# Kernel tuning notes

Measured on AMD Instinct MI355X. Metric: run time of the kernel, lower is better.

The kernel has to match this reference:

```python
import jax, jax.numpy as jnp
import numpy as np

S = 32          # input grid resolution
N = 2048        # active input voxels
C = 256         # in channels
CO = 128        # out channels
S2 = 2 * S      # upsampled resolution
M = 8 * N       # candidate child voxels
EPS = 1e-6


def setup_inputs() -> dict:
    key = jax.random.key(0)
    ks = jax.random.split(key, 8)
    # unique voxel coordinates (sparse occupancy)
    lin = jax.random.permutation(ks[0], S ** 3)[:N]
    coords = jnp.stack([lin // (S * S), (lin // S) % S, lin % S], axis=-1).astype(jnp.int32)
    sc = 0.05
    return {
        "feats": jax.random.normal(ks[1], (N, C), jnp.float32),
        "norm1_w": 1.0 + 0.1 * jax.random.normal(ks[2], (C,), jnp.float32),
        "norm1_b": 0.1 * jax.random.normal(ks[3], (C,), jnp.float32),
        "subdiv_w": sc * jax.random.normal(ks[4], (C, 8), jnp.float32),
        "subdiv_b": jnp.zeros((8,), jnp.float32),
        "conv1_w": sc * jax.random.normal(ks[5], (27, C, CO), jnp.float32),
        "conv1_b": jnp.zeros((CO,), jnp.float32),
        "conv2_w": sc * jax.random.normal(ks[6], (27, CO, CO), jnp.float32),
        "conv2_b": jnp.zeros((CO,), jnp.float32),
        "skip_w": sc * jax.random.normal(ks[7], (C, CO), jnp.float32),
        "skip_b": jnp.zeros((CO,), jnp.float32),
        "coords": coords,
    }


def _layernorm(x, w=None, b=None):
    # LayerNorm32: fp32 math, eps=1e-6
    m = jnp.mean(x, axis=-1, keepdims=True)
    v = jnp.var(x, axis=-1, keepdims=True)
    y = (x - m) * jax.lax.rsqrt(v + EPS)
    if w is not None:
        y = y * w + b
    return y


def _sparse_conv(feats, nidx, w, b):
    # submanifold 3x3x3 sparse conv: gather 27 neighbors, contract.
    # nidx: [M,27] with sentinel M pointing at a zero row.
    pad = jnp.concatenate([feats, jnp.zeros((1, feats.shape[1]), feats.dtype)], axis=0)
    g = pad[nidx]                                   # [M, 27, Cin]
    return jnp.einsum('nkc,kcd->nd', g, w) + b


def _forward(feats, norm1_w, norm1_b, subdiv_w, subdiv_b, conv1_w, conv1_b,
             conv2_w, conv2_b, skip_w, skip_b, coords):
    # subdiv prediction (SparseLinear C -> 8)
    subdiv = feats @ subdiv_w + subdiv_b            # [N, 8]
    # norm1 + silu
    h = jax.nn.silu(_layernorm(feats, norm1_w, norm1_b))
    # sparse upsample x2 with octree subdivision mask
    mask = (subdiv > 0).reshape(-1)                 # [M]
    j = jnp.arange(8, dtype=jnp.int32)
    offs8 = jnp.stack([(j >> 2) & 1, (j >> 1) & 1, j & 1], axis=-1)  # [8,3]
    cc = (coords[:, None, :] * 2 + offs8[None]).reshape(-1, 3)        # [M,3]
    h_c = jnp.where(mask[:, None], jnp.repeat(h, 8, axis=0), 0.0)     # [M,C]
    x_c = jnp.where(mask[:, None], jnp.repeat(feats, 8, axis=0), 0.0)
    # neighbor lookup grid (padded by 1; default M -> zero feature row)
    grid = jnp.full((S2 + 2, S2 + 2, S2 + 2), M, jnp.int32)
    grid = grid.at[cc[:, 0] + 1, cc[:, 1] + 1, cc[:, 2] + 1].set(
        jnp.arange(M, dtype=jnp.int32))
    d = jnp.arange(-1, 2, dtype=jnp.int32)
    offs27 = jnp.stack(jnp.meshgrid(d, d, d, indexing='ij'), axis=-1).reshape(27, 3)
    nc = cc[:, None, :] + 1 + offs27[None]          # [M,27,3]
    nidx = grid[nc[..., 0], nc[..., 1], nc[..., 2]] # [M,27]
    # conv1 -> norm2 (no affine) -> silu -> conv2
    h1 = jax.nn.silu(_layernorm(_sparse_conv(h_c, nidx, conv1_w, conv1_b)))
    h2 = _sparse_conv(h1, nidx, conv2_w, conv2_b)
    # residual with linear skip; mask out non-subdivided children
    out = (h2 + x_c @ skip_w + skip_b) * mask[:, None].astype(h2.dtype)
    return out, subdiv


def reference(feats, norm1_w, norm1_b, subdiv_w, subdiv_b, conv1_w, conv1_b,
              conv2_w, conv2_b, skip_w, skip_b, coords):
    return _forward(feats, norm1_w, norm1_b, subdiv_w, subdiv_b, conv1_w,
                    conv1_b, conv2_w, conv2_b, skip_w, skip_b, coords)
```

## Files before the change

kernel.cpp:

```cpp
#include <hip/hip_runtime.h>
#include <cstdint>
#include <cstddef>

constexpr int N  = 2048;
constexpr int C  = 256;
constexpr int CO = 128;
constexpr int M  = 16384;
constexpr int G  = 66;
constexpr int KP = 4;
constexpr int KCHUNK = 7;
constexpr float EPS = 1e-6f;

using bf8 = __attribute__((ext_vector_type(8))) short;
using f4  = __attribute__((ext_vector_type(4))) float;

#define AS1 __attribute__((address_space(1)))
#define AS3 __attribute__((address_space(3)))

static __device__ __forceinline__ void gl_lds16(const void* g, void* l) {
  __builtin_amdgcn_global_load_lds((AS1 const void*)g, (AS3 void*)l, 16, 0, 0);
}

static __device__ __forceinline__ unsigned short f2bf(float f) {
  unsigned u = __float_as_uint(f);
  u += 0x7fffu + ((u >> 16) & 1u);
  return (unsigned short)(u >> 16);
}

__global__ void k_init(int* __restrict__ grid, unsigned short* __restrict__ h,
                       unsigned short* __restrict__ h1) {
  int i = blockIdx.x * 256 + threadIdx.x;
  if (i < G * G * G) grid[i] = M;
  if (i < C)  h[(size_t)N * C + i] = 0;
  if (i < CO) h1[(size_t)M * CO + i] = 0;
}

template <int CIN>
__global__ void k_wt(const float* __restrict__ w, unsigned short* __restrict__ wt) {
  int i = blockIdx.x * 256 + threadIdx.x;
  if (i >= 27 * CIN * CO) return;
  int c = i % CIN;
  int rest = i / CIN;
  int o = rest % CO;
  int k = rest / CO;
  wt[i] = f2bf(w[((size_t)(k * CIN + c)) * CO + o]);
}

__global__ __launch_bounds__(256) void k_rownorm(
    const float* __restrict__ feats, const float* __restrict__ n1w,
    const float* __restrict__ n1b, const float* __restrict__ sdw,
    const float* __restrict__ sdb, float* __restrict__ out_subdiv,
    unsigned short* __restrict__ h, int* __restrict__ pidx,
    float* __restrict__ maskf) {
  int n = blockIdx.x, t = threadIdx.x;
  float x = feats[(size_t)n * C + t];
  float4 w0 = *(const float4*)(sdw + t * 8);
  float4 w1 = *(const float4*)(sdw + t * 8 + 4);
  float v[10] = {x * w0.x, x * w0.y, x * w0.z, x * w0.w,
                 x * w1.x, x * w1.y, x * w1.z, x * w1.w, x, x * x};
#pragma unroll
  for (int mk = 1; mk < 64; mk <<= 1) {
#pragma unroll
    for (int j = 0; j < 10; ++j) v[j] += __shfl_xor(v[j], mk, 64);
  }
  __shared__ float red[4][10];
  int wave = t >> 6, lane = t & 63;
  if (lane == 0) {
#pragma unroll
    for (int j = 0; j < 10; ++j) red[wave][j] = v[j];
  }
  __syncthreads();
  float sums[10];
#pragma unroll
  for (int j = 0; j < 10; ++j)
    sums[j] = red[0][j] + red[1][j] + red[2][j] + red[3][j];
  float mean = sums[8] / (float)C;
  float var  = sums[9] / (float)C - mean * mean;
  float rstd = rsqrtf(var + EPS);
  if (t < 8) {
    float sd = sums[t] + sdb[t];
    out_subdiv[(size_t)n * 8 + t] = sd;
    bool mk = sd > 0.f;
    pidx[n * 8 + t]  = mk ? n : N;
    maskf[n * 8 + t] = mk ? 1.f : 0.f;
  }
  float y  = (x - mean) * rstd * n1w[t] + n1b[t];
  float sl = y / (1.f + __expf(-y));
  h[(size_t)n * C + t] = f2bf(sl);
}

__global__ void k_scatter(const int* __restrict__ coords, int* __restrict__ grid) {
  int m = blockIdx.x * 256 + threadIdx.x;
  if (m >= M) return;
  int p = m >> 3, j = m & 7;
  int x = coords[p * 3 + 0] * 2 + ((j >> 2) & 1) + 1;
  int y = coords[p * 3 + 1] * 2 + ((j >> 1) & 1) + 1;
  int z = coords[p * 3 + 2] * 2 + (j & 1) + 1;
  grid[(x * G + y) * G + z] = m;
}

__global__ void k_nidx(const int* __restrict__ coords, const int* __restrict__ grid,
                       const int* __restrict__ pidx, int* __restrict__ nidxt,
                       int* __restrict__ g1t) {
  int idx = blockIdx.x * 256 + threadIdx.x;
  if (idx >= M * 27) return;
  int m = idx & (M - 1);
  int k = idx >> 14;
  int p = m >> 3, j = m & 7;
  int dx = k / 9 - 1;
  int dy = (k / 3) % 3 - 1;
  int dz = k % 3 - 1;
  int x = coords[p * 3 + 0] * 2 + ((j >> 2) & 1) + 1 + dx;
  int y = coords[p * 3 + 1] * 2 + ((j >> 1) & 1) + 1 + dy;
  int z = coords[p * 3 + 2] * 2 + (j & 1) + 1 + dz;
  int gv = grid[(x * G + y) * G + z];
  nidxt[idx] = gv;
  g1t[idx] = (gv == M) ? N : pidx[gv];
}

__global__ __launch_bounds__(256) void k_skip(const float* __restrict__ feats,
                                              const float* __restrict__ skw,
                                              const float* __restrict__ skb,
                                              float* __restrict__ s) {
  __shared__ float tile[32][36];
  int t = threadIdx.x;
  int rb = (blockIdx.x >> 1) * 32;
  int ob = (blockIdx.x & 1) * 64;
  int o = ob + (t & 63);
  int rg = (t >> 6) * 8;
  float acc[8] = {0, 0, 0, 0, 0, 0, 0, 0};
  for (int cb = 0; cb < C; cb += 32) {
    __syncthreads();
    int row = t >> 3, cc = (t & 7) * 4;
    *(float4*)&tile[row][cc] =
        *(const float4*)(feats + (size_t)(rb + row) * C + cb + cc);
    __syncthreads();
    for (int c = 0; c < 32; ++c) {
      float wv = skw[(size_t)(cb + c) * CO + o];
#pragma unroll
      for (int r = 0; r < 8; ++r) acc[r] += tile[rg + r][c] * wv;
    }
  }
  float bv = skb[o];
#pragma unroll
  for (int r = 0; r < 8; ++r) s[(size_t)(rb + rg + r) * CO + o] = acc[r] + bv;
}

template <int CIN, int NCB>
__global__ __launch_bounds__(256) void k_conv(
    const unsigned short* __restrict__ src, const int* __restrict__ gt,
    const unsigned short* __restrict__ wt, float* __restrict__ part) {
  __shared__ unsigned short sA[2][128 * 64];
  __shared__ unsigned short sB[2][128 * 64];
  const int t = threadIdx.x;
  const int w = t >> 6, lane = t & 63;
  const int quad = lane >> 4, ln = lane & 15;
  const int m0 = blockIdx.x * 128;
  const int kpart = blockIdx.y;
  const int k0 = kpart * KCHUNK;
  const int nk = min(KCHUNK, 27 - k0);
  const int nstage = nk * NCB;
  const int rh = (w >> 1) * 64, ch = (w & 1) * 64;

  const int sr = lane >> 3;
  const int gc = (lane & 7) ^ sr;

  auto stage = [&](int s, int buf) {
    const int kk = k0 + s / NCB;
    const int cb = s - (s / NCB) * NCB;
    const int colbase = cb * 64 + gc * 8;
    const int* gk = gt + (size_t)kk * M + m0;
#pragma unroll
    for (int tt = 0; tt < 4; ++tt) {
      const int seg = w * 4 + tt;
      const int r = seg * 8 + sr;
      const int ga = gk[r];
      gl_lds16(src + (size_t)ga * CIN + colbase, &sA[buf][seg * 512]);
      gl_lds16(wt + ((size_t)kk * CO + r) * CIN + colbase, &sB[buf][seg * 512]);
    }
  };

  f4 acc[16];
  f4 zero = {0.f, 0.f, 0.f, 0.f};
#pragma unroll
  for (int i = 0; i < 16; ++i) acc[i] = zero;

  stage(0, 0);
  for (int s = 0; s < nstage; ++s) {
    __syncthreads();
    if (s + 1 < nstage) stage(s + 1, (s + 1) & 1);
    const unsigned short* pa = sA[s & 1];
    const unsigned short* pb = sB[s & 1];
#pragma unroll
    for (int kc = 0; kc < 2; ++kc) {
      bf8 av[4], bv[4];
#pragma unroll
      for (int ti = 0; ti < 4; ++ti) {
        int row = rh + ti * 16 + ln;
        int sc = (kc * 4 + quad) ^ (row & 7);
        av[ti] = *(const bf8*)(pa + row * 64 + sc * 8);
      }
#pragma unroll
      for (int tj = 0; tj < 4; ++tj) {
        int row = ch + tj * 16 + ln;
        int sc = (kc * 4 + quad) ^ (row & 7);
        bv[tj] = *(const bf8*)(pb + row * 64 + sc * 8);
      }
#pragma unroll
      for (int ti = 0; ti < 4; ++ti)
#pragma unroll
        for (int tj = 0; tj < 4; ++tj)
          acc[ti * 4 + tj] = __builtin_amdgcn_mfma_f32_16x16x32_bf16(
              av[ti], bv[tj], acc[ti * 4 + tj], 0, 0, 0);
    }
  }

  float* pp = part + ((size_t)kpart * M + m0) * CO;
#pragma unroll
  for (int ti = 0; ti < 4; ++ti) {
    int mrow = rh + ti * 16 + quad * 4;
#pragma unroll
    for (int tj = 0; tj < 4; ++tj) {
      int co = ch + tj * 16 + ln;
#pragma unroll
      for (int rr = 0; rr < 4; ++rr)
        pp[(size_t)(mrow + rr) * CO + co] = acc[ti * 4 + tj][rr];
    }
  }
}

__global__ __launch_bounds__(256) void k_r1(const float* __restrict__ p,
                                            const float* __restrict__ bias,
                                            unsigned short* __restrict__ h1) {
  int wave = threadIdx.x >> 6, lane = threadIdx.x & 63;
  int m = blockIdx.x * 4 + wave;
  float v0 = bias[lane], v1 = bias[lane + 64];
#pragma unroll
  for (int q = 0; q < KP; ++q) {
    const float* pq = p + ((size_t)q * M + m) * CO;
    v0 += pq[lane];
    v1 += pq[lane + 64];
  }
  float sum = v0 + v1, sq = v0 * v0 + v1 * v1;
#pragma unroll
  for (int mk = 1; mk < 64; mk <<= 1) {
    sum += __shfl_xor(sum, mk, 64);
    sq  += __shfl_xor(sq, mk, 64);
  }
  float mean = sum / (float)CO;
  float var  = sq / (float)CO - mean * mean;
  float rstd = rsqrtf(var + EPS);
  float y0 = (v0 - mean) * rstd;
  float y1 = (v1 - mean) * rstd;
  float s0 = y0 / (1.f + __expf(-y0));
  float s1 = y1 / (1.f + __expf(-y1));
  h1[(size_t)m * CO + lane]      = f2bf(s0);
  h1[(size_t)m * CO + lane + 64] = f2bf(s1);
}

__global__ __launch_bounds__(256) void k_r2(const float* __restrict__ p,
                                            const float* __restrict__ bias,
                                            const float* __restrict__ sres,
                                            const float* __restrict__ maskf,
                                            float* __restrict__ out) {
  int i = blockIdx.x * 256 + threadIdx.x;
  int m = i >> 5;
  int o4 = (i & 31) * 4;
  float4 acc = *(const float4*)(bias + o4);
#pragma unroll
  for (int q = 0; q < KP; ++q) {
    float4 a = *(const float4*)(p + ((size_t)q * M + m) * CO + o4);
    acc.x += a.x; acc.y += a.y; acc.z += a.z; acc.w += a.w;
  }
  float4 s = *(const float4*)(sres + (size_t)(m >> 3) * CO + o4);
  float mk = maskf[m];
  float4 r;
  r.x = (acc.x + s.x) * mk;
  r.y = (acc.y + s.y) * mk;
  r.z = (acc.z + s.z) * mk;
  r.w = (acc.w + s.w) * mk;
  *(float4*)(out + (size_t)m * CO + o4) = r;
}

extern "C" void kernel_launch(void* const* d_in, const int* in_sizes, int n_in,
                              void* d_out, int out_size, void* d_ws, size_t ws_size,
                              hipStream_t stream) {
  const float* feats = (const float*)d_in[0];
  const float* n1w   = (const float*)d_in[1];
  const float* n1b   = (const float*)d_in[2];
  const float* sdw   = (const float*)d_in[3];
  const float* sdb   = (const float*)d_in[4];
  const float* c1w   = (const float*)d_in[5];
  const float* c1b   = (const float*)d_in[6];
  const float* c2w   = (const float*)d_in[7];
  const float* c2b   = (const float*)d_in[8];
  const float* skw   = (const float*)d_in[9];
  const float* skb   = (const float*)d_in[10];
  const int* coords  = (const int*)d_in[11];
  float* out = (float*)d_out;

  char* ws = (char*)d_ws;
  size_t off = 0;
  auto alloc = [&](size_t bytes) -> char* {
    char* p = ws + off;
    off += (bytes + 255) & ~(size_t)255;
    return p;
  };
  unsigned short* h    = (unsigned short*)alloc((size_t)(N + 1) * C * 2);
  unsigned short* h1   = (unsigned short*)alloc((size_t)(M + 1) * CO * 2);
  int*   grid  = (int*)alloc((size_t)G * G * G * 4);
  int*   nidxt = (int*)alloc((size_t)27 * M * 4);
  int*   g1t   = (int*)alloc((size_t)27 * M * 4);
  int*   pidx  = (int*)alloc((size_t)M * 4);
  float* maskf = (float*)alloc((size_t)M * 4);
  float* sres  = (float*)alloc((size_t)N * CO * 4);
  unsigned short* w1t = (unsigned short*)alloc((size_t)27 * CO * C * 2);
  unsigned short* w2t = (unsigned short*)alloc((size_t)27 * CO * CO * 2);
  float* pc = (float*)alloc((size_t)KP * M * CO * 4);

  k_init<<<(G * G * G + 255) / 256, 256, 0, stream>>>(grid, h, h1);
  k_wt<C><<<(27 * C * CO + 255) / 256, 256, 0, stream>>>(c1w, w1t);
  k_wt<CO><<<(27 * CO * CO + 255) / 256, 256, 0, stream>>>(c2w, w2t);
  k_rownorm<<<N, 256, 0, stream>>>(feats, n1w, n1b, sdw, sdb,
                                   out + (size_t)M * CO, h, pidx, maskf);
  k_scatter<<<(M + 255) / 256, 256, 0, stream>>>(coords, grid);
  k_nidx<<<(M * 27 + 255) / 256, 256, 0, stream>>>(coords, grid, pidx, nidxt, g1t);
  k_skip<<<128, 256, 0, stream>>>(feats, skw, skb, sres);

  k_conv<C, 4><<<dim3(M / 128, KP), 256, 0, stream>>>(h, g1t, w1t, pc);
  k_r1<<<M / 4, 256, 0, stream>>>(pc, c1b, h1);

  k_conv<CO, 2><<<dim3(M / 128, KP), 256, 0, stream>>>(h1, nidxt, w2t, pc);
  k_r2<<<M * CO / 4 / 256, 256, 0, stream>>>(pc, c2b, sres, maskf, out);
}
```

Baseline: 209.8 us.

## Shrink conv K-tile to 32, split kernel offsets seven ways, preload gather indices

The conv kernel now stages 32-wide K slices instead of 64, which halves LDS per block and, together with a launch bound of 4 blocks per CU, aims for higher occupancy. The 27 kernel offsets are split into 7 partitions of 4 instead of 4 of 7, giving more blocks across the GPU. Gather indices are loaded into registers once at kernel start rather than on every stage, and the LDS swizzle is reworked for the narrower tile. In exchange there are twice as many stage/sync iterations, more partial-sum traffic (7 partials written and reduced instead of 4), and more register pressure from the index array.

```diff
diff --git a/kernel.cpp b/kernel.cpp
--- a/kernel.cpp
+++ b/kernel.cpp
@@ -7,8 +7,8 @@
 constexpr int CO = 128;
 constexpr int M  = 16384;
 constexpr int G  = 66;
-constexpr int KP = 4;
-constexpr int KCHUNK = 7;
+constexpr int KP = 7;
+constexpr int KCHUNK = 4;
 constexpr float EPS = 1e-6f;
 
 using bf8 = __attribute__((ext_vector_type(8))) short;
@@ -147,11 +147,11 @@
 }
 
 template <int CIN, int NCB>
-__global__ __launch_bounds__(256) void k_conv(
+__global__ __launch_bounds__(256, 4) void k_conv(
     const unsigned short* __restrict__ src, const int* __restrict__ gt,
     const unsigned short* __restrict__ wt, float* __restrict__ part) {
-  __shared__ unsigned short sA[2][128 * 64];
-  __shared__ unsigned short sB[2][128 * 64];
+  __shared__ unsigned short sA[2][128 * 32];
+  __shared__ unsigned short sB[2][128 * 32];
   const int t = threadIdx.x;
   const int w = t >> 6, lane = t & 63;
   const int quad = lane >> 4, ln = lane & 15;
@@ -162,21 +162,35 @@
   const int nstage = nk * NCB;
   const int rh = (w >> 1) * 64, ch = (w & 1) * 64;
 
-  const int sr = lane >> 3;
-  const int gc = (lane & 7) ^ sr;
+  const int srow = lane >> 2;
+  const int gchunk = (lane & 3) ^ ((lane >> 3) & 3);
+
+  int ga[KCHUNK][2];
+#pragma unroll
+  for (int kk = 0; kk < KCHUNK; ++kk) {
+#pragma unroll
+    for (int rr = 0; rr < 2; ++rr) {
+      ga[kk][rr] = (kk < nk)
+          ? gt[(size_t)(k0 + kk) * M + m0 + rr * 64 + w * 16 + (lane >> 2)]
+          : 0;
+    }
+  }
+  (void)srow;
 
   auto stage = [&](int s, int buf) {
-    const int kk = k0 + s / NCB;
-    const int cb = s - (s / NCB) * NCB;
-    const int colbase = cb * 64 + gc * 8;
-    const int* gk = gt + (size_t)kk * M + m0;
-#pragma unroll
-    for (int tt = 0; tt < 4; ++tt) {
-      const int seg = w * 4 + tt;
-      const int r = seg * 8 + sr;
-      const int ga = gk[r];
-      gl_lds16(src + (size_t)ga * CIN + colbase, &sA[buf][seg * 512]);
-      gl_lds16(wt + ((size_t)kk * CO + r) * CIN + colbase, &sB[buf][seg * 512]);
+    const int kk = s / NCB;
+    const int cb = s - kk * NCB;
+    const int colbase = cb * 32 + gchunk * 8;
+#pragma unroll
+    for (int rr = 0; rr < 2; ++rr) {
+      gl_lds16(src + (size_t)ga[kk][rr] * CIN + colbase,
+               &sA[buf][(rr * 64 + w * 16) * 32]);
+    }
+#pragma unroll
+    for (int rr = 0; rr < 2; ++rr) {
+      const int corow = rr * 64 + w * 16 + (lane >> 2);
+      gl_lds16(wt + ((size_t)(k0 + kk) * CO + corow) * CIN + colbase,
+               &sB[buf][(rr * 64 + w * 16) * 32]);
     }
   };
 
@@ -184,6 +198,8 @@
   f4 zero = {0.f, 0.f, 0.f, 0.f};
 #pragma unroll
   for (int i = 0; i < 16; ++i) acc[i] = zero;
+
+  const int slot = quad ^ ((ln >> 1) & 3);
 
   stage(0, 0);
   for (int s = 0; s < nstage; ++s) {
@@ -191,28 +207,23 @@
     if (s + 1 < nstage) stage(s + 1, (s + 1) & 1);
     const unsigned short* pa = sA[s & 1];
     const unsigned short* pb = sB[s & 1];
-#pragma unroll
-    for (int kc = 0; kc < 2; ++kc) {
-      bf8 av[4], bv[4];
-#pragma unroll
-      for (int ti = 0; ti < 4; ++ti) {
-        int row = rh + ti * 16 + ln;
-        int sc = (kc * 4 + quad) ^ (row & 7);
-        av[ti] = *(const bf8*)(pa + row * 64 + sc * 8);
-      }
-#pragma unroll
-      for (int tj = 0; tj < 4; ++tj) {
-        int row = ch + tj * 16 + ln;
-        int sc = (kc * 4 + quad) ^ (row & 7);
-        bv[tj] = *(const bf8*)(pb + row * 64 + sc * 8);
-      }
-#pragma unroll
-      for (int ti = 0; ti < 4; ++ti)
-#pragma unroll
-        for (int tj = 0; tj < 4; ++tj)
-          acc[ti * 4 + tj] = __builtin_amdgcn_mfma_f32_16x16x32_bf16(
-              av[ti], bv[tj], acc[ti * 4 + tj], 0, 0, 0);
-    }
+    bf8 av[4], bv[4];
+#pragma unroll
+    for (int ti = 0; ti < 4; ++ti) {
+      int row = rh + ti * 16 + ln;
+      av[ti] = *(const bf8*)(pa + row * 32 + slot * 8);
+    }
+#pragma unroll
+    for (int tj = 0; tj < 4; ++tj) {
+      int row = ch + tj * 16 + ln;
+      bv[tj] = *(const bf8*)(pb + row * 32 + slot * 8);
+    }
+#pragma unroll
+    for (int ti = 0; ti < 4; ++ti)
+#pragma unroll
+      for (int tj = 0; tj < 4; ++tj)
+        acc[ti * 4 + tj] = __builtin_amdgcn_mfma_f32_16x16x32_bf16(
+            av[ti], bv[tj], acc[ti * 4 + tj], 0, 0, 0);
   }
 
   float* pp = part + ((size_t)kpart * M + m0) * CO;
@@ -327,9 +338,9 @@
   k_nidx<<<(M * 27 + 255) / 256, 256, 0, stream>>>(coords, grid, pidx, nidxt, g1t);
   k_skip<<<128, 256, 0, stream>>>(feats, skw, skb, sres);
 
-  k_conv<C, 4><<<dim3(M / 128, KP), 256, 0, stream>>>(h, g1t, w1t, pc);
+  k_conv<C, 8><<<dim3(M / 128, KP), 256, 0, stream>>>(h, g1t, w1t, pc);
   k_r1<<<M / 4, 256, 0, stream>>>(pc, c1b, h1);
 
-  k_conv<CO, 2><<<dim3(M / 128, KP), 256, 0, stream>>>(h1, nidxt, w2t, pc);
+  k_conv<CO, 4><<<dim3(M / 128, KP), 256, 0, stream>>>(h1, nidxt, w2t, pc);
   k_r2<<<M * CO / 4 / 256, 256, 0, stream>>>(pc, c2b, sres, maskf, out);
 }
```

After: 206.4 us. About the same (-1.6%).
